# Optimization experiments

Hardware: AMD Instinct MI355X
Metric: run time of the kernel (lower is better)

The kernel has to match this reference:

```python
import jax, jax.numpy as jnp
import numpy as np

SEP_THRESHOLD = 5.0
TEMPERATURE = 0.1          # sigmoid temperature
SCALING_FACTOR = 1.0
DIST_TEMPERATURE = 1.0     # exponential temperature for repulsion energy
ATT_LOSS_GATE = 0.0
REP_LOSS_GATE = 0.0
EPS = 1e-10


def setup_inputs() -> dict:
    key = jax.random.key(0)
    k1, k2 = jax.random.split(key)
    B, L, K, C, D = 16, 64, 32, 32, 512
    prior = jax.random.normal(k1, (B, L, K, C), dtype=jnp.float32)
    h = jax.random.normal(k2, (B, L, D), dtype=jnp.float32)
    return {"prior": prior, "h": h}


def _jsd_matrix(prior):
    # prior: (B, L, K, C) logits -> pairwise JSD summed over K factors: (B, L, L)
    logp = jax.nn.log_softmax(prior, axis=-1)          # (B,L,K,C)
    p = jnp.exp(logp)
    p1, p2 = p[:, :, None], p[:, None]                  # (B,L,1,K,C), (B,1,L,K,C)
    lp1, lp2 = logp[:, :, None], logp[:, None]
    logm = jnp.log(0.5 * (p1 + p2))                     # mixture log-probs
    kl_p_m = jnp.sum(p1 * (lp1 - logm), axis=-1)        # (B,L,L,K)
    kl_q_m = jnp.sum(p2 * (lp2 - logm), axis=-1)
    jsd = 0.5 * (kl_p_m + kl_q_m)
    return jsd.sum(axis=-1) * SCALING_FACTOR            # (B,L,L)


def _ste_mask(soft, hard, triu):
    # straight-through: hard values forward, soft gradient backward
    return (hard + soft - jax.lax.stop_gradient(soft)) * triu


def reference(prior, h):
    B, L, K, C = prior.shape
    jsd = _jsd_matrix(prior)                            # (B,L,L)

    triu = jnp.triu(jnp.ones((L, L), dtype=prior.dtype), k=1)
    soft_att = jax.nn.sigmoid((SEP_THRESHOLD - jsd) / TEMPERATURE)
    hard_att = (jsd < SEP_THRESHOLD).astype(prior.dtype)
    att_mask = _ste_mask(soft_att, hard_att, triu)
    soft_rep = jax.nn.sigmoid((jsd - SEP_THRESHOLD) / TEMPERATURE)
    hard_rep = (jsd >= SEP_THRESHOLD).astype(prior.dtype)
    rep_mask = _ste_mask(soft_rep, hard_rep, triu)

    # pairwise MSE over hidden dim: (B,L,L)
    diff = h[:, :, None, :] - h[:, None, :, :]
    pairwise_mse = jnp.mean(diff * diff, axis=-1)

    loss_att = (pairwise_mse * att_mask).sum() / (att_mask.sum() + EPS)
    loss_att = jnp.where(loss_att > ATT_LOSS_GATE, loss_att, 0.0)

    repulsion_energy = jnp.exp(-pairwise_mse / DIST_TEMPERATURE)
    loss_rep = (repulsion_energy * rep_mask).sum() / (rep_mask.sum() + EPS)
    loss_rep = jnp.where(loss_rep > REP_LOSS_GATE, loss_rep, 0.0)

    return loss_att, loss_rep
```

## Files before the change

### kernel.cpp

```cpp
#include <hip/hip_runtime.h>
#include <math.h>

#define NB 16
#define NL 64
#define NK 32
#define NC 32
#define ND 512
#define EPSF 1e-10f

#define TILES_PER_B 36
#define PAIR_BLOCKS (NB * TILES_PER_B * 2)

#define THRS 14.426950408889634f
#define L2E  1.4426950408889634f

typedef _Float16 half2v __attribute__((ext_vector_type(2)));
typedef _Float16 half4v __attribute__((ext_vector_type(4)));
typedef _Float16 half8v __attribute__((ext_vector_type(8)));


__global__ void __launch_bounds__(256) softmax_kernel(
        const float* __restrict__ prior,
        const float* __restrict__ hg,
        _Float16* __restrict__ P,
        float2* __restrict__ H2,
        _Float16* __restrict__ h16) {
    int bl = blockIdx.x;
    int t  = threadIdx.x;

    const float* src = prior + (size_t)bl * (NK * NC);
    float4 x = *(const float4*)(src + t * 4);
    float y0 = x.x * L2E, y1 = x.y * L2E, y2 = x.z * L2E, y3 = x.w * L2E;

    float m = fmaxf(fmaxf(y0, y1), fmaxf(y2, y3));
    #pragma unroll
    for (int w = 4; w >= 1; w >>= 1)
        m = fmaxf(m, __shfl_xor(m, w, 8));

    float e0 = exp2f(y0 - m), e1 = exp2f(y1 - m);
    float e2 = exp2f(y2 - m), e3 = exp2f(y3 - m);
    float s = e0 + e1 + e2 + e3;
    #pragma unroll
    for (int w = 4; w >= 1; w >>= 1)
        s += __shfl_xor(s, w, 8);

    float rs = 1.0f / s;
    float ls = __log2f(s);
    float p0 = e0 * rs, p1 = e1 * rs, p2 = e2 * rs, p3 = e3 * rs;
    float l0 = (y0 - m) - ls, l1 = (y1 - m) - ls;
    float l2 = (y2 - m) - ls, l3 = (y3 - m) - ls;

    half4v pv;
    pv[0] = (_Float16)fmaxf(p0, 1e-6f);
    pv[1] = (_Float16)fmaxf(p1, 1e-6f);
    pv[2] = (_Float16)fmaxf(p2, 1e-6f);
    pv[3] = (_Float16)fmaxf(p3, 1e-6f);
    *(half4v*)(P + (size_t)bl * (NK * NC) + t * 4) = pv;

    float2 hv = *(const float2*)(hg + (size_t)bl * ND + t * 2);
    half2v hh; hh[0] = (_Float16)hv.x; hh[1] = (_Float16)hv.y;
    *(half2v*)(h16 + (size_t)bl * ND + t * 2) = hh;

    float hacc = p0 * l0 + p1 * l1 + p2 * l2 + p3 * l3;
    #pragma unroll
    for (int w = 32; w >= 1; w >>= 1)
        hacc += __shfl_xor(hacc, w);
    __shared__ float red[4];
    int lane = t & 63, wib = t >> 6;
    if (lane == 0) red[wib] = hacc;
    __syncthreads();
    if (t == 0)
        H2[bl] = make_float2(red[0] + red[1], red[2] + red[3]);
}

__device__ __forceinline__ float bf4(float v0, float v1, float v2, float v3,
                                     bool hi32, bool hi16) {
    float sel0 = hi32 ? v2 : v0, oth0 = hi32 ? v0 : v2;
    float sel1 = hi32 ? v3 : v1, oth1 = hi32 ? v1 : v3;
    float w0 = sel0 + __shfl_xor(oth0, 32);
    float w1 = sel1 + __shfl_xor(oth1, 32);
    float sel = hi16 ? w1 : w0, oth = hi16 ? w0 : w1;
    float x = sel + __shfl_xor(oth, 16);
    x += __shfl_xor(x, 8);
    x += __shfl_xor(x, 4);
    x += __shfl_xor(x, 2);
    x += __shfl_xor(x, 1);
    return x;
}

__global__ void __launch_bounds__(256) pair_kernel(
        const _Float16* __restrict__ P,
        const float2* __restrict__ H2g,
        const _Float16* __restrict__ h16,
        float* __restrict__ partials) {
    __shared__ float red[4][4];

    int tid  = threadIdx.x;
    int lane = tid & 63;
    int wv   = tid >> 6;

    int wg    = blockIdx.x;
    int b     = wg / (TILES_PER_B * 2);
    int rem72 = wg % (TILES_PER_B * 2);
    int t36   = rem72 >> 1;
    int half  = rem72 & 1;

    int ti = 0, rem = t36;
    while (rem >= 8 - ti) { rem -= 8 - ti; ++ti; }
    int tj = ti + rem;
    bool diag = (ti == tj);
    int bi0 = b * NL + ti * 8;
    int bj0 = b * NL + tj * 8;

    int r = half * 4 + wv;

    const _Float16* arow = P + (size_t)(bi0 + r) * (NK * NC);
    half8v ar1 = *(const half8v*)(arow + lane * 8);
    half8v ar2 = *(const half8v*)(arow + 512 + lane * 8);
    half8v hr  = *(const half8v*)(h16 + (size_t)(bi0 + r) * ND + lane * 8);
    float2 h2i = H2g[bi0 + r];

    const _Float16* Pj = P   + (size_t)bj0 * (NK * NC);
    const _Float16* Hj = h16 + (size_t)bj0 * ND;

    bool hi32 = (lane & 32) != 0;
    bool hi16 = (lane & 16) != 0;
    int  sgrp = lane >> 4;

    float attN = 0.0f, attC = 0.0f, repN = 0.0f, repC = 0.0f;

    #pragma unroll
    for (int sb = 0; sb < 8; sb += 4) {
        float S[4], M[4];
        #pragma unroll
        for (int q = 0; q < 4; ++q) {
            int s = sb + q;
            half8v b1 = *(const half8v*)(Pj + s * 1024 + lane * 8);
            half8v t1 = ar1 + b1;
            float a0 = 0.f, a1 = 0.f;
            #pragma unroll
            for (int e = 0; e < 8; e += 2) {
                float f0 = (float)t1[e];     a0 = fmaf(f0, __log2f(f0), a0);
                float f1 = (float)t1[e + 1]; a1 = fmaf(f1, __log2f(f1), a1);
            }
            S[q] = a0 + a1;

            half8v hs = *(const half8v*)(Hj + s * 512 + lane * 8);
            half8v d = hr - hs;
            float m0 = 0.f, m1 = 0.f;
            #pragma unroll
            for (int e = 0; e < 8; e += 2) {
                m0 = fmaf((float)d[e],     (float)d[e],     m0);
                m1 = fmaf((float)d[e + 1], (float)d[e + 1], m1);
            }
            M[q] = m0 + m1;
        }

        float xSA = bf4(S[0], S[1], S[2], S[3], hi32, hi16);
        float xM  = bf4(M[0], M[1], M[2], M[3], hi32, hi16);

        int smine = sb + sgrp;
        float2 h2j = H2g[bj0 + smine];
        float statA = h2i.x + h2j.x + 32.0f - xSA;
        bool valid = (!diag) || (smine > r);
        float stat = statA;

        if (__any(valid && (statA < THRS))) {
            float SB[4];
            #pragma unroll
            for (int q = 0; q < 4; ++q) {
                int s = sb + q;
                half8v b2 = *(const half8v*)(Pj + s * 1024 + 512 + lane * 8);
                half8v t2 = ar2 + b2;
                float a0 = 0.f, a1 = 0.f;
                #pragma unroll
                for (int e = 0; e < 8; e += 2) {
                    float g0 = (float)t2[e];     a0 = fmaf(g0, __log2f(g0), a0);
                    float g1 = (float)t2[e + 1]; a1 = fmaf(g1, __log2f(g1), a1);
                }
                SB[q] = a0 + a1;
            }
            float xSB = bf4(SB[0], SB[1], SB[2], SB[3], hi32, hi16);
            stat = statA + (h2i.y + h2j.y + 32.0f - xSB);
        }

        float mse   = xM * (1.0f / ND);
        float rterm = exp2f(-mse * L2E);
        bool act   = ((lane & 15) == 0) && valid;
        bool isAtt = stat < THRS;
        attN += (act && isAtt)  ? mse   : 0.0f;
        attC += (act && isAtt)  ? 1.0f  : 0.0f;
        repN += (act && !isAtt) ? rterm : 0.0f;
        repC += (act && !isAtt) ? 1.0f  : 0.0f;
    }

    attN += __shfl_xor(attN, 16); attN += __shfl_xor(attN, 32);
    attC += __shfl_xor(attC, 16); attC += __shfl_xor(attC, 32);
    repN += __shfl_xor(repN, 16); repN += __shfl_xor(repN, 32);
    repC += __shfl_xor(repC, 16); repC += __shfl_xor(repC, 32);

    if (lane == 0) {
        red[wv][0] = attN; red[wv][1] = attC;
        red[wv][2] = repN; red[wv][3] = repC;
    }
    __syncthreads();
    if (tid < 4) {
        float v = red[0][tid] + red[1][tid] + red[2][tid] + red[3][tid];
        partials[blockIdx.x * 4 + tid] = v;
    }
}

__global__ void __launch_bounds__(256) finalize_kernel(
        const float* __restrict__ partials,
        float* __restrict__ out) {
    int tid = threadIdx.x;
    float a0 = 0.0f, a1 = 0.0f, a2 = 0.0f, a3 = 0.0f;
    for (int bkt = tid; bkt < PAIR_BLOCKS; bkt += 256) {
        a0 += partials[bkt * 4 + 0];
        a1 += partials[bkt * 4 + 1];
        a2 += partials[bkt * 4 + 2];
        a3 += partials[bkt * 4 + 3];
    }
    #pragma unroll
    for (int w = 32; w >= 1; w >>= 1) {
        a0 += __shfl_xor(a0, w);
        a1 += __shfl_xor(a1, w);
        a2 += __shfl_xor(a2, w);
        a3 += __shfl_xor(a3, w);
    }
    __shared__ float red[4][4];
    int lane = tid & 63, wib = tid >> 6;
    if (lane == 0) {
        red[wib][0] = a0; red[wib][1] = a1; red[wib][2] = a2; red[wib][3] = a3;
    }
    __syncthreads();
    if (tid == 0) {
        float s0 = red[0][0] + red[1][0] + red[2][0] + red[3][0];
        float s1 = red[0][1] + red[1][1] + red[2][1] + red[3][1];
        float s2 = red[0][2] + red[1][2] + red[2][2] + red[3][2];
        float s3 = red[0][3] + red[1][3] + red[2][3] + red[3][3];
        float la = s0 / (s1 + EPSF);
        float lr = s2 / (s3 + EPSF);
        out[0] = (la > 0.0f) ? la : 0.0f;
        out[1] = (lr > 0.0f) ? lr : 0.0f;
    }
}

extern "C" void kernel_launch(void* const* d_in, const int* in_sizes, int n_in,
                              void* d_out, int out_size, void* d_ws, size_t ws_size,
                              hipStream_t stream) {
    const float* prior = (const float*)d_in[0];
    const float* h     = (const float*)d_in[1];
    float* out = (float*)d_out;
    float* ws  = (float*)d_ws;

    float* partials = ws;
    _Float16* P = (_Float16*)(ws + 8192);
    float2* H2 = (float2*)(ws + 8192 + 524288);
    _Float16* h16 = (_Float16*)(ws + 8192 + 524288 + 2048);

    softmax_kernel<<<NB * NL, 256, 0, stream>>>(prior, h, P, H2, h16);

    pair_kernel<<<PAIR_BLOCKS, 256, 0, stream>>>(P, H2, h16, partials);

    finalize_kernel<<<1, 256, 0, stream>>>(partials, out);
}
```

Baseline: 24.26 us.

## Split pair work across more blocks, drop early-exit, use DPP reductions

Doubles the pair grid so each wave handles one row against four columns, with each lane covering 16 contiguous probabilities so all 32 factors are summed in one pass. This removes the two-stage JSD with its wave-vote early exit and the outer sb loop. The final intra-16-lane shuffle steps become DPP row_shr adds, with results read from lane 15 of each group. The entropy term H2 is collapsed to a single float. Every pair now always evaluates the full JSD, which trades the skipped second half for more parallelism and shorter per-wave latency.

```diff
diff --git a/kernel.cpp b/kernel.cpp
--- a/kernel.cpp
+++ b/kernel.cpp
@@ -9,7 +9,7 @@
 #define EPSF 1e-10f
 
 #define TILES_PER_B 36
-#define PAIR_BLOCKS (NB * TILES_PER_B * 2)
+#define PAIR_BLOCKS (NB * TILES_PER_B * 4)
 
 #define THRS 14.426950408889634f
 #define L2E  1.4426950408889634f
@@ -23,7 +23,7 @@
         const float* __restrict__ prior,
         const float* __restrict__ hg,
         _Float16* __restrict__ P,
-        float2* __restrict__ H2,
+        float* __restrict__ H2,
         _Float16* __restrict__ h16) {
     int bl = blockIdx.x;
     int t  = threadIdx.x;
@@ -69,28 +69,33 @@
     int lane = t & 63, wib = t >> 6;
     if (lane == 0) red[wib] = hacc;
     __syncthreads();
-    if (t == 0)
-        H2[bl] = make_float2(red[0] + red[1], red[2] + red[3]);
-}
-
-__device__ __forceinline__ float bf4(float v0, float v1, float v2, float v3,
-                                     bool hi32, bool hi16) {
+    if (t == 0) H2[bl] = red[0] + red[1] + red[2] + red[3];
+}
+
+template<int CTRL>
+__device__ __forceinline__ float dpp_add(float x) {
+    int yi = __builtin_amdgcn_update_dpp(0, __float_as_int(x), CTRL, 0xF, 0xF, true);
+    return x + __int_as_float(yi);
+}
+
+__device__ __forceinline__ float bf4f(float v0, float v1, float v2, float v3,
+                                      bool hi32, bool hi16) {
     float sel0 = hi32 ? v2 : v0, oth0 = hi32 ? v0 : v2;
     float sel1 = hi32 ? v3 : v1, oth1 = hi32 ? v1 : v3;
     float w0 = sel0 + __shfl_xor(oth0, 32);
     float w1 = sel1 + __shfl_xor(oth1, 32);
     float sel = hi16 ? w1 : w0, oth = hi16 ? w0 : w1;
     float x = sel + __shfl_xor(oth, 16);
-    x += __shfl_xor(x, 8);
-    x += __shfl_xor(x, 4);
-    x += __shfl_xor(x, 2);
-    x += __shfl_xor(x, 1);
+    x = dpp_add<0x111>(x);
+    x = dpp_add<0x112>(x);
+    x = dpp_add<0x114>(x);
+    x = dpp_add<0x118>(x);
     return x;
 }
 
 __global__ void __launch_bounds__(256) pair_kernel(
         const _Float16* __restrict__ P,
-        const float2* __restrict__ H2g,
+        const float* __restrict__ H2g,
         const _Float16* __restrict__ h16,
         float* __restrict__ partials) {
     __shared__ float red[4][4];
@@ -99,11 +104,11 @@
     int lane = tid & 63;
     int wv   = tid >> 6;
 
-    int wg    = blockIdx.x;
-    int b     = wg / (TILES_PER_B * 2);
-    int rem72 = wg % (TILES_PER_B * 2);
-    int t36   = rem72 >> 1;
-    int half  = rem72 & 1;
+    int wg     = blockIdx.x;
+    int b      = wg / (TILES_PER_B * 4);
+    int rem144 = wg % (TILES_PER_B * 4);
+    int t36    = rem144 >> 2;
+    int quad   = rem144 & 3;
 
     int ti = 0, rem = t36;
     while (rem >= 8 - ti) { rem -= 8 - ti; ++ti; }
@@ -112,94 +117,74 @@
     int bi0 = b * NL + ti * 8;
     int bj0 = b * NL + tj * 8;
 
-    int r = half * 4 + wv;
-
-    const _Float16* arow = P + (size_t)(bi0 + r) * (NK * NC);
-    half8v ar1 = *(const half8v*)(arow + lane * 8);
-    half8v ar2 = *(const half8v*)(arow + 512 + lane * 8);
+    int r    = quad * 2 + (wv >> 1);
+    int scol = (wv & 1) * 4;
+
+    const _Float16* arow = P + (size_t)(bi0 + r) * (NK * NC) + lane * 16;
+    half8v arA = *(const half8v*)(arow);
+    half8v arB = *(const half8v*)(arow + 8);
     half8v hr  = *(const half8v*)(h16 + (size_t)(bi0 + r) * ND + lane * 8);
-    float2 h2i = H2g[bi0 + r];
-
-    const _Float16* Pj = P   + (size_t)bj0 * (NK * NC);
-    const _Float16* Hj = h16 + (size_t)bj0 * ND;
+    float h2i = H2g[bi0 + r];
+
+    const _Float16* Pj = P   + (size_t)bj0 * (NK * NC) + lane * 16;
+    const _Float16* Hj = h16 + (size_t)bj0 * ND + lane * 8;
 
     bool hi32 = (lane & 32) != 0;
     bool hi16 = (lane & 16) != 0;
     int  sgrp = lane >> 4;
-
-    float attN = 0.0f, attC = 0.0f, repN = 0.0f, repC = 0.0f;
-
-    #pragma unroll
-    for (int sb = 0; sb < 8; sb += 4) {
-        float S[4], M[4];
+    bool actl = (lane & 15) == 15;
+
+    float S[4], M[4];
+    #pragma unroll
+    for (int q = 0; q < 4; ++q) {
+        int s = scol + q;
+        const _Float16* brow = Pj + s * 1024;
+        half8v b0 = *(const half8v*)(brow);
+        half8v b1 = *(const half8v*)(brow + 8);
+        half8v t0 = arA + b0;
+        half8v t1 = arB + b1;
+        float a0 = 0.f, a1 = 0.f, a2 = 0.f, a3 = 0.f;
         #pragma unroll
-        for (int q = 0; q < 4; ++q) {
-            int s = sb + q;
-            half8v b1 = *(const half8v*)(Pj + s * 1024 + lane * 8);
-            half8v t1 = ar1 + b1;
-            float a0 = 0.f, a1 = 0.f;
-            #pragma unroll
-            for (int e = 0; e < 8; e += 2) {
-                float f0 = (float)t1[e];     a0 = fmaf(f0, __log2f(f0), a0);
-                float f1 = (float)t1[e + 1]; a1 = fmaf(f1, __log2f(f1), a1);
-            }
-            S[q] = a0 + a1;
-
-            half8v hs = *(const half8v*)(Hj + s * 512 + lane * 8);
-            half8v d = hr - hs;
-            float m0 = 0.f, m1 = 0.f;
-            #pragma unroll
-            for (int e = 0; e < 8; e += 2) {
-                m0 = fmaf((float)d[e],     (float)d[e],     m0);
-                m1 = fmaf((float)d[e + 1], (float)d[e + 1], m1);
-            }
-            M[q] = m0 + m1;
+        for (int e = 0; e < 8; e += 2) {
+            float f0 = (float)t0[e];     a0 = fmaf(f0, __log2f(f0), a0);
+            float f1 = (float)t0[e + 1]; a1 = fmaf(f1, __log2f(f1), a1);
+            float g0 = (float)t1[e];     a2 = fmaf(g0, __log2f(g0), a2);
+            float g1 = (float)t1[e + 1]; a3 = fmaf(g1, __log2f(g1), a3);
         }
-
-        float xSA = bf4(S[0], S[1], S[2], S[3], hi32, hi16);
-        float xM  = bf4(M[0], M[1], M[2], M[3], hi32, hi16);
-
-        int smine = sb + sgrp;
-        float2 h2j = H2g[bj0 + smine];
-        float statA = h2i.x + h2j.x + 32.0f - xSA;
-        bool valid = (!diag) || (smine > r);
-        float stat = statA;
-
-        if (__any(valid && (statA < THRS))) {
-            float SB[4];
-            #pragma unroll
-            for (int q = 0; q < 4; ++q) {
-                int s = sb + q;
-                half8v b2 = *(const half8v*)(Pj + s * 1024 + 512 + lane * 8);
-                half8v t2 = ar2 + b2;
-                float a0 = 0.f, a1 = 0.f;
-                #pragma unroll
-                for (int e = 0; e < 8; e += 2) {
-                    float g0 = (float)t2[e];     a0 = fmaf(g0, __log2f(g0), a0);
-                    float g1 = (float)t2[e + 1]; a1 = fmaf(g1, __log2f(g1), a1);
-                }
-                SB[q] = a0 + a1;
-            }
-            float xSB = bf4(SB[0], SB[1], SB[2], SB[3], hi32, hi16);
-            stat = statA + (h2i.y + h2j.y + 32.0f - xSB);
+        S[q] = (a0 + a1) + (a2 + a3);
+
+        half8v hs = *(const half8v*)(Hj + s * 512);
+        half8v d = hr - hs;
+        float m0 = 0.f, m1 = 0.f;
+        #pragma unroll
+        for (int e = 0; e < 8; e += 2) {
+            m0 = fmaf((float)d[e],     (float)d[e],     m0);
+            m1 = fmaf((float)d[e + 1], (float)d[e + 1], m1);
         }
-
-        float mse   = xM * (1.0f / ND);
-        float rterm = exp2f(-mse * L2E);
-        bool act   = ((lane & 15) == 0) && valid;
-        bool isAtt = stat < THRS;
-        attN += (act && isAtt)  ? mse   : 0.0f;
-        attC += (act && isAtt)  ? 1.0f  : 0.0f;
-        repN += (act && !isAtt) ? rterm : 0.0f;
-        repC += (act && !isAtt) ? 1.0f  : 0.0f;
-    }
+        M[q] = m0 + m1;
+    }
+
+    float xS = bf4f(S[0], S[1], S[2], S[3], hi32, hi16);
+    float xM = bf4f(M[0], M[1], M[2], M[3], hi32, hi16);
+
+    int s = scol + sgrp;
+    float stat = h2i + H2g[bj0 + s] + 64.0f - xS;
+    float mse  = xM * (1.0f / ND);
+    float rt   = exp2f(-mse * L2E);
+    bool valid = (!diag) || (s > r);
+    bool isAtt = stat < THRS;
+
+    float attN = (actl && valid && isAtt)  ? mse : 0.f;
+    float attC = (actl && valid && isAtt)  ? 1.f : 0.f;
+    float repN = (actl && valid && !isAtt) ? rt  : 0.f;
+    float repC = (actl && valid && !isAtt) ? 1.f : 0.f;
 
     attN += __shfl_xor(attN, 16); attN += __shfl_xor(attN, 32);
     attC += __shfl_xor(attC, 16); attC += __shfl_xor(attC, 32);
     repN += __shfl_xor(repN, 16); repN += __shfl_xor(repN, 32);
     repC += __shfl_xor(repC, 16); repC += __shfl_xor(repC, 32);
 
-    if (lane == 0) {
+    if (lane == 63) {
         red[wv][0] = attN; red[wv][1] = attC;
         red[wv][2] = repN; red[wv][3] = repC;
     }
@@ -255,9 +240,9 @@
     float* ws  = (float*)d_ws;
 
     float* partials = ws;
-    _Float16* P = (_Float16*)(ws + 8192);
-    float2* H2 = (float2*)(ws + 8192 + 524288);
-    _Float16* h16 = (_Float16*)(ws + 8192 + 524288 + 2048);
+    _Float16* P = (_Float16*)(ws + 16384);
+    float* H2 = ws + 16384 + 524288;
+    _Float16* h16 = (_Float16*)(ws + 16384 + 524288 + 1024);
 
     softmax_kernel<<<NB * NL, 256, 0, stream>>>(prior, h, P, H2, h16);
 
```

After: 23.62 us. -2.6%, faster.
